# Optimization experiments

Hardware: AMD Instinct MI355X
Metric: run time of the kernel (lower is better)

Reference implementation:

```python
import jax, jax.numpy as jnp
import numpy as np

B, C, N_OUT = 8, 64, 65536
N_IN = 262144  # unpooled (input) spatial size
K, P = 9, 4    # kernel_size, bilinear interp points


def setup_inputs() -> dict:
    key = jax.random.key(0)
    k1, k2, k3, k4 = jax.random.split(key, 4)
    x = jax.random.normal(k1, (B, C, N_OUT), dtype=jnp.float32)
    idx_mask = jax.random.randint(k2, (B, C, N_OUT), 0, K, dtype=jnp.int32)
    sample_map = jax.random.randint(k3, (N_OUT, K, P), 0, N_IN, dtype=jnp.int32)
    interp_weights = jax.random.uniform(k4, (N_OUT, K, P), dtype=jnp.float32)
    return {"x": x, "idx_mask": idx_mask, "sample_map": sample_map,
            "interp_weights": interp_weights}


def reference(x, idx_mask, sample_map, interp_weights):
    # x: [B,C,N_out] pooled values; idx_mask: [B,C,N_out] winning kernel tap
    # sample_map: [N_out,K,P] int indices into flattened unpooled domain
    # interp_weights: [N_out,K,P] interpolation weights
    b, c, n_out = x.shape
    o_idx = jnp.arange(n_out)[None, None, :]               # [1,1,N_out]
    sel_map = sample_map[o_idx, idx_mask]                  # [B,C,N_out,P]
    sel_w = interp_weights[o_idx, idx_mask]                # [B,C,N_out,P]
    contrib = sel_w * x[..., None]                         # [B,C,N_out,P]
    out = jnp.zeros((b, c, N_IN), dtype=x.dtype)
    bi = jnp.arange(b)[:, None, None, None]
    ci = jnp.arange(c)[None, :, None, None]
    out = out.at[bi, ci, sel_map].add(contrib)             # scatter-add unpool
    return out
```

## Files before the change

### kernel.cpp

```cpp
#include <hip/hip_runtime.h>

#define BB      8
#define CC      64
#define N_OUT   65536
#define N_IN    262144
#define KK      9
#define PP      4
#define NE      (N_OUT * KK * PP)
#define NPLANES 512
#define CHUNK   32
#define NCHUNKS (N_IN / CHUNK)
#define GTH     512
#define NW      (GTH / 64)

#define WS_COUNTS  0
#define WS_CURSOR  8192
#define WS_OFFSETS 16384
#define WS_HDR     24640
#define WS_ENTR    614464
#define WS_XK      10051648
#define WS_END     43606080

__global__ __launch_bounds__(256) void k_zero_ints(int* __restrict__ p, int n4) {
    int i = blockIdx.x * 256 + threadIdx.x;
    int stride = gridDim.x * 256;
    const int4 z = {0, 0, 0, 0};
    for (; i < n4; i += stride) ((int4*)p)[i] = z;
}

#define XKTILE 16
#define XPAD   520
__global__ __launch_bounds__(256) void k_xk(const float* __restrict__ x,
                                            const int*   __restrict__ idx,
                                            unsigned* __restrict__ xk,
                                            unsigned* __restrict__ hdr) {
    __shared__ float xs[XKTILE * XPAD];
    __shared__ unsigned char ks[XKTILE * XPAD];
    __shared__ unsigned ot[XKTILE * 512];
    __shared__ int cnt[XKTILE][12];
    __shared__ int cur[XKTILE][12];
    const int t = threadIdx.x;
    const int obase = blockIdx.x * XKTILE;

    for (int i = t; i < XKTILE * 12; i += 256) cnt[i / 12][i % 12] = 0;

    for (int i = t; i < 512 * (XKTILE / 4); i += 256) {
        int p = i >> 2, q = i & 3;
        const size_t g = (size_t)p * N_OUT + obase + 4 * q;
        float4 xv = *(const float4*)(x + g);
        int4   kv = *(const int4*)(idx + g);
        int b = (4 * q) * XPAD + p;
        xs[b] = xv.x; xs[b + XPAD] = xv.y; xs[b + 2 * XPAD] = xv.z; xs[b + 3 * XPAD] = xv.w;
        ks[b] = (unsigned char)kv.x; ks[b + XPAD] = (unsigned char)kv.y;
        ks[b + 2 * XPAD] = (unsigned char)kv.z; ks[b + 3 * XPAD] = (unsigned char)kv.w;
    }
    __syncthreads();
    for (int i = t; i < XKTILE * 512; i += 256) {
        int oo = i >> 9, p = i & 511;
        atomicAdd(&cnt[oo][ks[oo * XPAD + p]], 1);
    }
    __syncthreads();
    if (t < XKTILE) {
        int s = 0;
        for (int k = 0; k < KK; ++k) {
            int c = cnt[t][k];
            cur[t][k] = s;
            hdr[(size_t)(obase + t) * KK + k] = (unsigned)(s | (c << 16));
            s += c;
        }
    }
    __syncthreads();
    for (int i = t; i < XKTILE * 512; i += 256) {
        int oo = i >> 9, p = i & 511;
        int k = ks[oo * XPAD + p];
        int pos = atomicAdd(&cur[oo][k], 1);
        unsigned xb = __float_as_uint(xs[oo * XPAD + p]);
        ot[(oo << 9) + pos] = (xb & 0xFFFFFE00u) | (unsigned)p;
    }
    __syncthreads();
    for (int i = t; i < XKTILE * 128; i += 256) {
        int oo = i >> 7, c4 = i & 127;
        ((int4*)(xk + (((size_t)(obase + oo)) << 9)))[c4] = ((const int4*)(ot + (oo << 9)))[c4];
    }
}

__global__ __launch_bounds__(256) void k_hist5(const int* __restrict__ smap,
                                               int* __restrict__ counts) {
    int e = blockIdx.x * 256 + threadIdx.x;
    if (e < NE) atomicAdd(&counts[smap[e] >> 5], 1);
}

__global__ __launch_bounds__(1024) void k_scan8k(const int* __restrict__ counts,
                                                 int* __restrict__ offsets) {
    __shared__ int sw[1024];
    const int t = threadIdx.x;
    int4 a = ((const int4*)counts)[2 * t];
    int4 b = ((const int4*)counts)[2 * t + 1];
    int s = a.x + a.y + a.z + a.w + b.x + b.y + b.z + b.w;
    sw[t] = s;
    __syncthreads();
    for (int off = 1; off < 1024; off <<= 1) {
        int v = (t >= off) ? sw[t - off] : 0;
        __syncthreads();
        sw[t] += v;
        __syncthreads();
    }
    int run = sw[t] - s;
    int vals[8] = {a.x, a.y, a.z, a.w, b.x, b.y, b.z, b.w};
    int o[8];
    #pragma unroll
    for (int q = 0; q < 8; ++q) { o[q] = run; run += vals[q]; }
    ((int4*)offsets)[2 * t]     = make_int4(o[0], o[1], o[2], o[3]);
    ((int4*)offsets)[2 * t + 1] = make_int4(o[4], o[5], o[6], o[7]);
    if (t == 1023) offsets[8192] = NE;
}

__global__ __launch_bounds__(256) void k_fill5(const int* __restrict__ smap,
                                               const float* __restrict__ wts,
                                               const int* __restrict__ offsets,
                                               int* __restrict__ cursor,
                                               const unsigned* __restrict__ hdr,
                                               int4* __restrict__ entries) {
    int e = blockIdx.x * 256 + threadIdx.x;
    if (e >= NE) return;
    int n = smap[e];
    int o = e / 36;
    int r = e - o * 36;
    int k = r >> 2;
    unsigned h = hdr[(size_t)o * KK + k];
    int key = n >> 5;
    int pos = offsets[key] + atomicAdd(&cursor[key], 1);
    entries[pos] = make_int4((o << 5) | (n & 31), __float_as_int(wts[e]), (int)h, 0);
}

__global__ __launch_bounds__(GTH) void k_gather5(const int* __restrict__ offsets,
                                                 const int4* __restrict__ entries,
                                                 const unsigned* __restrict__ xk,
                                                 float* __restrict__ out) {
    __shared__ float acc[CHUNK * NPLANES];
    const int c = blockIdx.x;
    const int tid = threadIdx.x;
    const int lane = tid & 63;
    const int wid = tid >> 6;

    float4* a4 = (float4*)acc;
    for (int i = tid; i < CHUNK * NPLANES / 4; i += GTH) a4[i] = float4{0.f, 0.f, 0.f, 0.f};
    __syncthreads();

    const int j1 = offsets[c + 1];
    int j = offsets[c] + wid;
    int4 e = make_int4(0, 0, 0, 0);
    unsigned u0 = 0;
    bool have = (j < j1);
    if (have) {
        e = entries[j];
        int o = ((unsigned)e.x) >> 5;
        int st = e.z & 0xFFFF;
        int cn = ((unsigned)e.z) >> 16;
        if (lane < cn) u0 = xk[((size_t)o << 9) + st + lane];
    }
    while (have) {
        const int jn = j + NW;
        const bool hn = (jn < j1);
        int4 en = make_int4(0, 0, 0, 0);
        unsigned un = 0;
        if (hn) {
            en = entries[jn];
            int on = ((unsigned)en.x) >> 5;
            int stn = en.z & 0xFFFF;
            int cnn = ((unsigned)en.z) >> 16;
            if (lane < cnn) un = xk[((size_t)on << 9) + stn + lane];
        }
        {
            const int nl = e.x & 31;
            const float w = __int_as_float(e.y);
            const int cn = ((unsigned)e.z) >> 16;
            if (lane < cn) {
                int p = u0 & 511;
                float xv = __int_as_float(u0 & 0xFFFFFE00u);
                atomicAdd(&acc[(nl << 9) + (p ^ nl)], w * xv);
            }
            if (cn > 64) {
                const int o = ((unsigned)e.x) >> 5;
                const int st = e.z & 0xFFFF;
                for (int b = lane + 64; b < cn; b += 64) {
                    unsigned u = xk[((size_t)o << 9) + st + b];
                    int p = u & 511;
                    float xv = __int_as_float(u & 0xFFFFFE00u);
                    atomicAdd(&acc[(nl << 9) + (p ^ nl)], w * xv);
                }
            }
        }
        e = en; u0 = un; j = jn; have = hn;
    }
    __syncthreads();

    const int n0 = c << 5;
    for (int i = tid; i < CHUNK * NPLANES; i += GTH) {
        int p = i >> 5, nl = i & 31;
        __builtin_nontemporal_store(acc[(nl << 9) + (p ^ nl)],
                                    out + (size_t)p * N_IN + n0 + nl);
    }
}

__global__ __launch_bounds__(256) void zero_kernel(float4* __restrict__ out, int n4) {
    int i = blockIdx.x * blockDim.x + threadIdx.x;
    int stride = gridDim.x * blockDim.x;
    const float4 z = {0.f, 0.f, 0.f, 0.f};
    for (; i < n4; i += stride) out[i] = z;
}

__global__ __launch_bounds__(256) void scatter_kernel(
    const float* __restrict__ x, const int* __restrict__ idx_mask,
    const int4* __restrict__ smap, const float4* __restrict__ wts,
    float* __restrict__ out)
{
    const int plane = blockIdx.x >> 8;
    const int o = ((blockIdx.x & 255) << 8) + threadIdx.x;
    const long ibase = (long)plane * N_OUT + o;
    const float xv = x[ibase];
    const int k = idx_mask[ibase];
    const int row = o * KK + k;
    const int4 m = smap[row];
    const float4 w = wts[row];
    float* op = out + (long)plane * N_IN;
    atomicAdd(op + m.x, w.x * xv);
    atomicAdd(op + m.y, w.y * xv);
    atomicAdd(op + m.z, w.z * xv);
    atomicAdd(op + m.w, w.w * xv);
}

extern "C" void kernel_launch(void* const* d_in, const int* in_sizes, int n_in,
                              void* d_out, int out_size, void* d_ws, size_t ws_size,
                              hipStream_t stream) {
    const float* x    = (const float*)d_in[0];
    const int*   idx  = (const int*)d_in[1];
    const int*   smap = (const int*)d_in[2];
    const float* wts  = (const float*)d_in[3];
    float* out = (float*)d_out;

    if (ws_size < (size_t)WS_END * 4) {
        zero_kernel<<<4096, 256, 0, stream>>>((float4*)out, out_size / 4);
        scatter_kernel<<<NPLANES * (N_OUT / 256), 256, 0, stream>>>(
            x, idx, (const int4*)smap, (const float4*)wts, out);
        return;
    }

    int* ws = (int*)d_ws;
    int* counts    = ws + WS_COUNTS;
    int* cursor    = ws + WS_CURSOR;
    int* offsets   = ws + WS_OFFSETS;
    unsigned* hdr  = (unsigned*)(ws + WS_HDR);
    int4* entries  = (int4*)(ws + WS_ENTR);
    unsigned* xk   = (unsigned*)(ws + WS_XK);

    k_zero_ints<<<16, 256, 0, stream>>>(counts, 16384 / 4);
    k_xk<<<N_OUT / XKTILE, 256, 0, stream>>>(x, idx, xk, hdr);
    k_hist5<<<NE / 256, 256, 0, stream>>>(smap, counts);
    k_scan8k<<<1, 1024, 0, stream>>>(counts, offsets);
    k_fill5<<<NE / 256, 256, 0, stream>>>(smap, wts, offsets, cursor, hdr, entries);
    k_gather5<<<NCHUNKS, GTH, 0, stream>>>(offsets, entries, xk, out);
}
```

Baseline: 1.090 ms.

## Use per-block LDS histograms for bucket sort and vectorize gather output stores

Replaces the global-atomic histogram and fill with 64 blocks that each build a private 8192-bin LDS histogram. A single-block scan then turns these into per-block cursors, and the fill step places entries using LDS atomics. This removes contended global atomics and the zeroing kernel. The gather kernel also remaps block order across chunks and writes output as float4 with normal stores instead of scalar nontemporal stores. The trade-off is that histogram and fill now run on only 64 blocks and the scan does serial per-key passes over 64 rows, which may limit parallelism.

After: 1.815 ms. +66.5%, slower.

```diff
diff --git a/kernel.cpp b/kernel.cpp
--- a/kernel.cpp
+++ b/kernel.cpp
@@ -12,21 +12,15 @@
 #define NCHUNKS (N_IN / CHUNK)
 #define GTH     512
 #define NW      (GTH / 64)
-
-#define WS_COUNTS  0
-#define WS_CURSOR  8192
-#define WS_OFFSETS 16384
-#define WS_HDR     24640
-#define WS_ENTR    614464
-#define WS_XK      10051648
-#define WS_END     43606080
-
-__global__ __launch_bounds__(256) void k_zero_ints(int* __restrict__ p, int n4) {
-    int i = blockIdx.x * 256 + threadIdx.x;
-    int stride = gridDim.x * 256;
-    const int4 z = {0, 0, 0, 0};
-    for (; i < n4; i += stride) ((int4*)p)[i] = z;
-}
+#define NFB     64
+#define EPB     (NE / NFB)
+
+#define WS_OFFSETS 0
+#define WS_PRIV    8208
+#define WS_HDR     (8208 + NFB * 8192)
+#define WS_ENTR    (532496 + N_OUT * KK)
+#define WS_XK      (1122320 + 4 * NE)
+#define WS_END     (10559504 + N_OUT * 512)
 
 #define XKTILE 16
 #define XPAD   520
@@ -84,20 +78,40 @@
     }
 }
 
-__global__ __launch_bounds__(256) void k_hist5(const int* __restrict__ smap,
-                                               int* __restrict__ counts) {
-    int e = blockIdx.x * 256 + threadIdx.x;
-    if (e < NE) atomicAdd(&counts[smap[e] >> 5], 1);
-}
-
-__global__ __launch_bounds__(1024) void k_scan8k(const int* __restrict__ counts,
-                                                 int* __restrict__ offsets) {
+__global__ __launch_bounds__(1024) void k_histA(const int* __restrict__ smap,
+                                                int* __restrict__ priv) {
+    __shared__ int h[8192];
+    const int b = blockIdx.x;
+    const int t = threadIdx.x;
+    for (int i = t; i < 8192; i += 1024) h[i] = 0;
+    __syncthreads();
+    const int e0 = b * EPB;
+    #pragma unroll 4
+    for (int i = 0; i < EPB / 1024; ++i)
+        atomicAdd(&h[smap[e0 + i * 1024 + t] >> 5], 1);
+    __syncthreads();
+    for (int i = t; i < 8192; i += 1024) priv[b * 8192 + i] = h[i];
+}
+
+__global__ __launch_bounds__(1024) void k_scanP(int* __restrict__ priv,
+                                                int* __restrict__ offsets) {
     __shared__ int sw[1024];
     const int t = threadIdx.x;
-    int4 a = ((const int4*)counts)[2 * t];
-    int4 b = ((const int4*)counts)[2 * t + 1];
-    int s = a.x + a.y + a.z + a.w + b.x + b.y + b.z + b.w;
-    sw[t] = s;
+    int tot[8];
+    #pragma unroll
+    for (int i = 0; i < 8; ++i) {
+        const int key = t * 8 + i;
+        int run = 0;
+        for (int b = 0; b < NFB; ++b) {
+            int* p = priv + b * 8192 + key;
+            int v = *p; *p = run; run += v;
+        }
+        tot[i] = run;
+    }
+    int myTot = 0;
+    #pragma unroll
+    for (int i = 0; i < 8; ++i) myTot += tot[i];
+    sw[t] = myTot;
     __syncthreads();
     for (int off = 1; off < 1024; off <<= 1) {
         int v = (t >= off) ? sw[t - off] : 0;
@@ -105,32 +119,40 @@
         sw[t] += v;
         __syncthreads();
     }
-    int run = sw[t] - s;
-    int vals[8] = {a.x, a.y, a.z, a.w, b.x, b.y, b.z, b.w};
-    int o[8];
-    #pragma unroll
-    for (int q = 0; q < 8; ++q) { o[q] = run; run += vals[q]; }
-    ((int4*)offsets)[2 * t]     = make_int4(o[0], o[1], o[2], o[3]);
-    ((int4*)offsets)[2 * t + 1] = make_int4(o[4], o[5], o[6], o[7]);
+    int base = sw[t] - myTot;
+    int kb[8];
+    #pragma unroll
+    for (int i = 0; i < 8; ++i) { kb[i] = base; base += tot[i]; }
+    #pragma unroll
+    for (int i = 0; i < 8; ++i) {
+        const int key = t * 8 + i;
+        offsets[key] = kb[i];
+        for (int b = 0; b < NFB; ++b) priv[b * 8192 + key] += kb[i];
+    }
     if (t == 1023) offsets[8192] = NE;
 }
 
-__global__ __launch_bounds__(256) void k_fill5(const int* __restrict__ smap,
-                                               const float* __restrict__ wts,
-                                               const int* __restrict__ offsets,
-                                               int* __restrict__ cursor,
-                                               const unsigned* __restrict__ hdr,
-                                               int4* __restrict__ entries) {
-    int e = blockIdx.x * 256 + threadIdx.x;
-    if (e >= NE) return;
-    int n = smap[e];
-    int o = e / 36;
-    int r = e - o * 36;
-    int k = r >> 2;
-    unsigned h = hdr[(size_t)o * KK + k];
-    int key = n >> 5;
-    int pos = offsets[key] + atomicAdd(&cursor[key], 1);
-    entries[pos] = make_int4((o << 5) | (n & 31), __float_as_int(wts[e]), (int)h, 0);
+__global__ __launch_bounds__(1024) void k_fillB(const int* __restrict__ smap,
+                                                const float* __restrict__ wts,
+                                                const int* __restrict__ priv,
+                                                const unsigned* __restrict__ hdr,
+                                                int4* __restrict__ entries) {
+    __shared__ int cur[8192];
+    const int b = blockIdx.x;
+    const int t = threadIdx.x;
+    for (int i = t; i < 8192; i += 1024) cur[i] = priv[b * 8192 + i];
+    __syncthreads();
+    const int e0 = b * EPB;
+    for (int i = 0; i < EPB / 1024; ++i) {
+        const int e = e0 + i * 1024 + t;
+        const int n = smap[e];
+        const int o = e / 36;
+        const int r = e - o * 36;
+        const int k = r >> 2;
+        const unsigned h = hdr[(size_t)o * KK + k];
+        const int pos = atomicAdd(&cur[n >> 5], 1);
+        entries[pos] = make_int4((o << 5) | (n & 31), __float_as_int(wts[e]), (int)h, 0);
+    }
 }
 
 __global__ __launch_bounds__(GTH) void k_gather5(const int* __restrict__ offsets,
@@ -138,7 +160,8 @@
                                                  const unsigned* __restrict__ xk,
                                                  float* __restrict__ out) {
     __shared__ float acc[CHUNK * NPLANES];
-    const int c = blockIdx.x;
+    const int bid = blockIdx.x;
+    const int c = (bid & 7) * (NCHUNKS / 8) + (bid >> 3);
     const int tid = threadIdx.x;
     const int lane = tid & 63;
     const int wid = tid >> 6;
@@ -196,10 +219,15 @@
     __syncthreads();
 
     const int n0 = c << 5;
-    for (int i = tid; i < CHUNK * NPLANES; i += GTH) {
-        int p = i >> 5, nl = i & 31;
-        __builtin_nontemporal_store(acc[(nl << 9) + (p ^ nl)],
-                                    out + (size_t)p * N_IN + n0 + nl);
+    for (int i = tid; i < CHUNK * NPLANES / 4; i += GTH) {
+        const int p = i >> 3;
+        const int nl = (i & 7) << 2;
+        float4 v;
+        v.x = acc[((nl + 0) << 9) + (p ^ (nl + 0))];
+        v.y = acc[((nl + 1) << 9) + (p ^ (nl + 1))];
+        v.z = acc[((nl + 2) << 9) + (p ^ (nl + 2))];
+        v.w = acc[((nl + 3) << 9) + (p ^ (nl + 3))];
+        *(float4*)(out + (size_t)p * N_IN + n0 + nl) = v;
     }
 }
 
@@ -247,17 +275,15 @@
     }
 
     int* ws = (int*)d_ws;
-    int* counts    = ws + WS_COUNTS;
-    int* cursor    = ws + WS_CURSOR;
     int* offsets   = ws + WS_OFFSETS;
+    int* priv      = ws + WS_PRIV;
     unsigned* hdr  = (unsigned*)(ws + WS_HDR);
     int4* entries  = (int4*)(ws + WS_ENTR);
     unsigned* xk   = (unsigned*)(ws + WS_XK);
 
-    k_zero_ints<<<16, 256, 0, stream>>>(counts, 16384 / 4);
     k_xk<<<N_OUT / XKTILE, 256, 0, stream>>>(x, idx, xk, hdr);
-    k_hist5<<<NE / 256, 256, 0, stream>>>(smap, counts);
-    k_scan8k<<<1, 1024, 0, stream>>>(counts, offsets);
-    k_fill5<<<NE / 256, 256, 0, stream>>>(smap, wts, offsets, cursor, hdr, entries);
+    k_histA<<<NFB, 1024, 0, stream>>>(smap, priv);
+    k_scanP<<<1, 1024, 0, stream>>>(priv, offsets);
+    k_fillB<<<NFB, 1024, 0, stream>>>(smap, wts, priv, hdr, entries);
     k_gather5<<<NCHUNKS, GTH, 0, stream>>>(offsets, entries, xk, out);
 }
```
